# Optimization experiments

Hardware: AMD Instinct MI355X
Metric: run time of the kernel (lower is better)

## Reference

```python
import jax, jax.numpy as jnp
import numpy as np
from jax import lax

EPS = 1e-5
DN = ('NCHW', 'OIHW', 'NCHW')


def _bn(x, gamma, beta, mean, var):
    # eval-mode BatchNorm2d over channel dim (axis=1)
    s = gamma / jnp.sqrt(var + EPS)
    return x * s[None, :, None, None] + (beta - mean * s)[None, :, None, None]


def setup_inputs() -> dict:
    key = jax.random.key(0)
    ks = jax.random.split(key, 12)
    B, Cin, C, H, W, NC = 128, 2048, 512, 14, 14, 200
    return {
        'feature': jax.random.normal(ks[0], (B, Cin, H, W), jnp.float32),
        'w_reduce': jax.random.normal(ks[1], (C, Cin, 1, 1), jnp.float32) * 0.02,
        'b_reduce': jax.random.normal(ks[2], (C,), jnp.float32) * 0.02,
        'bn1_gamma': jnp.ones((C,), jnp.float32),
        'bn1_beta': jnp.zeros((C,), jnp.float32),
        'bn1_mean': jax.random.normal(ks[3], (C,), jnp.float32) * 0.02,
        'bn1_var': jax.random.uniform(ks[4], (C,), jnp.float32),
        'w3': jax.random.normal(ks[5], (C, C, 3, 3), jnp.float32) * 0.02,
        'b3': jax.random.normal(ks[6], (C,), jnp.float32) * 0.02,
        'bn2_gamma': jnp.ones((C,), jnp.float32),
        'bn2_beta': jnp.zeros((C,), jnp.float32),
        'bn2_mean': jax.random.normal(ks[7], (C,), jnp.float32) * 0.02,
        'bn2_var': jax.random.uniform(ks[8], (C,), jnp.float32),
        'fc1_w': jax.random.normal(ks[9], (NC, C), jnp.float32) * 0.02,
        'fc1_b': jnp.zeros((NC,), jnp.float32),
        'fc2_w': jax.random.normal(ks[10], (NC, NC), jnp.float32) * 0.02,
        'fc2_b': jnp.zeros((NC,), jnp.float32),
    }


def reference(feature, w_reduce, b_reduce, bn1_gamma, bn1_beta, bn1_mean, bn1_var,
              w3, b3, bn2_gamma, bn2_beta, bn2_mean, bn2_var,
              fc1_w, fc1_b, fc2_w, fc2_b):
    B, _, H, W = feature.shape
    C = w_reduce.shape[0]  # 512
    # reduce: 1x1 conv + BN + ReLU
    f = lax.conv_general_dilated(feature, w_reduce, (1, 1), 'VALID', dimension_numbers=DN)
    f = f + b_reduce[None, :, None, None]
    f = jax.nn.relu(_bn(f, bn1_gamma, bn1_beta, bn1_mean, bn1_var))
    x = f.reshape(B, C, H * W)  # [B, 512, 196]
    # channel affinity + softmax(-xxt) over last dim (= the per-row loop)
    xxt = jnp.einsum('bcn,bdn->bcd', x, x)  # [B, 512, 512]
    a = jax.nn.softmax(-xxt, axis=2)
    y = jnp.einsum('bcd,bdn->bcn', a, x).reshape(B, C, H, W)
    # conv3: 3x3 conv + BN + ReLU + global avg pool
    z = lax.conv_general_dilated(y, w3, (1, 1), 'SAME', dimension_numbers=DN)
    z = z + b3[None, :, None, None]
    z = jax.nn.relu(_bn(z, bn2_gamma, bn2_beta, bn2_mean, bn2_var))
    z = jnp.mean(z, axis=(2, 3))  # [B, 512]
    # fc_channel: Linear -> ReLU -> Linear
    h = jax.nn.relu(z @ fc1_w.T + fc1_b)
    sf = h @ fc2_w.T + fc2_b
    return sf
```

## Files before the change

### kernel.cpp

```cpp
#include <hip/hip_runtime.h>

typedef __attribute__((ext_vector_type(8))) short bf16x8;
typedef __attribute__((ext_vector_type(4))) float f32x4;
typedef __attribute__((ext_vector_type(4))) short short4v;
typedef __attribute__((ext_vector_type(2))) short short2v;

__device__ __forceinline__ unsigned short f2bf(float x){
  unsigned u = __float_as_uint(x);
  return (unsigned short)((u + 0x7FFFu + ((u>>16)&1u)) >> 16);
}
__device__ __forceinline__ float bf2f(unsigned short b){
  return __uint_as_float(((unsigned)b)<<16);
}

typedef const __attribute__((address_space(1))) void* gas_t;
typedef __attribute__((address_space(3))) void* las_t;
__device__ __forceinline__ void gl16(const void* g, void* l){
  __builtin_amdgcn_global_load_lds((gas_t)g, (las_t)l, 16, 0, 0);
}

static constexpr size_t O_FHI  = 0;
static constexpr size_t O_FLO  = 102760448;
static constexpr size_t O_XHI  = 205520896;
static constexpr size_t O_XLO  = 239075328;
static constexpr size_t O_XT   = 272629760;
static constexpr size_t O_AMAT = 301989888;
static constexpr size_t O_WH   = 369098752;
static constexpr size_t O_WL   = 371195904;
static constexpr size_t O_W3B  = 373293056;
static constexpr size_t O_PAR  = 378011648;
static constexpr size_t O_FC1T = 378019840;
static constexpr size_t O_FC2T = 378429440;
static constexpr size_t O_ZBAR = 378589440;

__global__ __launch_bounds__(256) void k_prep(
    const float* wr, unsigned short* wh, unsigned short* wl,
    const float* w3, unsigned short* w3c,
    const float* fc1w, float* fc1T, const float* fc2w, float* fc2T,
    const float* br, const float* g1, const float* be1, const float* m1, const float* v1,
    const float* b3, const float* g2, const float* be2, const float* m2, const float* v2,
    float* par, unsigned short* xhi, unsigned short* xlo){
  int blk = blockIdx.x, t = threadIdx.x;
  if (blk < 4096){
    int idx = blk*256 + t;
    int c = idx >> 11, k = idx & 2047;
    float v = wr[(size_t)c*2048 + k];
    unsigned short h = f2bf(v);
    wh[(size_t)c*2048+k] = h; wl[(size_t)c*2048+k] = f2bf(v - bf2f(h));
  } else if (blk < 13312){
    int i = (blk-4096)*256 + t;
    int co = i / 4608, k = i - co*4608;
    int ci0b = k / 576, r2 = k - ci0b*576;
    int tap = r2 >> 6, cio = r2 & 63;
    w3c[(((size_t)ci0b*9+tap)*512+co)*64+cio] =
        f2bf(w3[((size_t)co*512 + ci0b*64+cio)*9 + tap]);
  } else if (blk < 13712){
    int i = (blk-13312)*256 + t;
    int k = i/200, j = i - k*200;
    fc1T[i] = fc1w[j*512+k];
  } else if (blk < 13869){
    int i = (blk-13712)*256 + t;
    if (i < 40000){ int k = i/200, j = i - k*200; fc2T[i] = fc2w[j*200+k]; }
  } else if (blk < 13871){
    int c = (blk-13869)*256 + t;
    if (c < 512){
      float s1 = g1[c]*rsqrtf(v1[c]+1e-5f);
      par[c] = s1; par[512+c] = (br[c]-m1[c])*s1 + be1[c];
      float s2 = g2[c]*rsqrtf(v2[c]+1e-5f);
      par[1024+c] = s2; par[1536+c] = (b3[c]-m2[c])*s2 + be2[c];
    }
  } else {
    int rr = (blk-13871)*256 + t;
    float4 z = {0.f,0.f,0.f,0.f};
    float4* a = (float4*)(xhi + (size_t)rr*256 + 192);
    float4* bq = (float4*)(xlo + (size_t)rr*256 + 192);
    #pragma unroll
    for (int q=0;q<8;++q){ a[q]=z; bq[q]=z; }
  }
}

__global__ __launch_bounds__(256) void k_featT(const float* __restrict__ feat,
        unsigned short* __restrict__ fhi, unsigned short* __restrict__ flo){
  __shared__ float tile[64][33];
  int b = blockIdx.z;
  int ci0 = blockIdx.y*64, p0 = blockIdx.x*32;
  int t = threadIdx.x;
  int j = t & 31, i0 = t >> 5;
  for (int rep=0; rep<8; ++rep){
    int i = rep*8 + i0;
    int p = p0 + j;
    tile[i][j] = (p<196) ? feat[((size_t)b*2048 + ci0 + i)*196 + p] : 0.f;
  }
  __syncthreads();
  int j2 = t & 31;
  int jj0 = t >> 5;
  for (int rep=0; rep<4; ++rep){
    int jj = rep*8 + jj0;
    int p = p0 + jj;
    if (p < 196){
      float v0 = tile[2*j2][jj], v1 = tile[2*j2+1][jj];
      unsigned short h0 = f2bf(v0), h1 = f2bf(v1);
      unsigned short l0 = f2bf(v0 - bf2f(h0)), l1 = f2bf(v1 - bf2f(h1));
      size_t o = ((size_t)b*196 + p)*2048 + ci0 + 2*j2;
      short2v hv; hv[0]=(short)h0; hv[1]=(short)h1;
      short2v lv; lv[0]=(short)l0; lv[1]=(short)l1;
      *(short2v*)(fhi + o) = hv;
      *(short2v*)(flo + o) = lv;
    }
  }
}

__global__ __launch_bounds__(256, 2) void k_conv1(
    const unsigned short* __restrict__ fhi, const unsigned short* __restrict__ flo,
    const unsigned short* __restrict__ wh,  const unsigned short* __restrict__ wl,
    const float* __restrict__ par,
    unsigned short* __restrict__ xhi, unsigned short* __restrict__ xlo,
    unsigned short* __restrict__ xT){
  __shared__ char lds[65536];
  char* BUF0 = lds;
  char* BUF1 = lds + 32768;
  int lin = blockIdx.x;
  int sz  = (lin&7)*98 + (lin>>3);
  int mt = sz&3;
  int gt = sz>>2;
  int c0 = mt*128;
  size_t g0 = (size_t)gt*128;
  int t = threadIdx.x, lane = t&63, wid = t>>6, wm = wid&1, wn = wid>>1;
  int fq = lane>>4, fr = lane&15;
  f32x4 acc[4][4] = {};

  auto STAGE = [&](int it, char* buf){
    #pragma unroll
    for (int jj=0; jj<8; ++jj){
      int arr = jj>>1;
      int g = t + ((jj&1)<<8);
      int row = g>>2;
      int cs = ((g&3) ^ ((row>>1)&3))*8;
      const unsigned short* src;
      if (arr==0)      src = wh  + (size_t)(c0+row)*2048 + it*32 + cs;
      else if (arr==1) src = wl  + (size_t)(c0+row)*2048 + it*32 + cs;
      else if (arr==2) src = fhi + (g0+row)*2048 + it*32 + cs;
      else             src = flo + (g0+row)*2048 + it*32 + cs;
      gl16(src, buf + arr*8192 + g*16);
    }
  };

  STAGE(0, BUF0);
  asm volatile("s_waitcnt vmcnt(0)" ::: "memory");
  __builtin_amdgcn_s_barrier();
  __builtin_amdgcn_sched_barrier(0);

  for (int it=0; it<64; ++it){
    char* cur = (it&1) ? BUF1 : BUF0;
    char* nxt = (it&1) ? BUF0 : BUF1;
    if (it < 63) STAGE(it+1, nxt);
    bf16x8 ah[4], al[4], bh[4], bl[4];
    #pragma unroll
    for (int m=0;m<4;++m){
      int row = wm*64 + m*16 + fr;
      int off = row*64 + ((fq*16) ^ (((row>>1)&3)<<4));
      ah[m] = *(const bf16x8*)(cur + off);
      al[m] = *(const bf16x8*)(cur + 8192 + off);
    }
    #pragma unroll
    for (int n=0;n<4;++n){
      int row = wn*64 + n*16 + fr;
      int off = row*64 + ((fq*16) ^ (((row>>1)&3)<<4));
      bh[n] = *(const bf16x8*)(cur + 16384 + off);
      bl[n] = *(const bf16x8*)(cur + 24576 + off);
    }
    __builtin_amdgcn_s_setprio(1);
    #pragma unroll
    for (int n=0;n<4;++n)
      #pragma unroll
      for (int m=0;m<4;++m){
        acc[m][n] = __builtin_amdgcn_mfma_f32_16x16x32_bf16(ah[m], bh[n], acc[m][n],0,0,0);
        acc[m][n] = __builtin_amdgcn_mfma_f32_16x16x32_bf16(ah[m], bl[n], acc[m][n],0,0,0);
        acc[m][n] = __builtin_amdgcn_mfma_f32_16x16x32_bf16(al[m], bh[n], acc[m][n],0,0,0);
      }
    __builtin_amdgcn_s_setprio(0);
    asm volatile("s_waitcnt vmcnt(0)" ::: "memory");
    __builtin_amdgcn_s_barrier();
    __builtin_amdgcn_sched_barrier(0);
  }

  const float* s1 = par; const float* t1 = par+512;
  for (int m=0;m<4;++m){
    int cb = c0 + wm*64 + m*16 + fq*4;
    float sc[4], sh[4];
    for (int j=0;j<4;++j){ sc[j]=s1[cb+j]; sh[j]=t1[cb+j]; }
    for (int n=0;n<4;++n){
      int gg = (int)g0 + wn*64 + n*16 + fr;
      int b = gg/196, p = gg - b*196;
      unsigned short hs[4];
      for (int j=0;j<4;++j){
        float v = fmaxf(acc[m][n][j]*sc[j]+sh[j], 0.f);
        unsigned short h = f2bf(v);
        hs[j] = h;
        size_t ic = (size_t)b*512 + cb + j;
        xhi[ic*256 + p] = h;
        xlo[ic*256 + p] = f2bf(v - bf2f(h));
      }
      *(short4v*)(xT + ((size_t)b*224 + p)*512 + cb) = *(short4v*)hs;
    }
  }
}

__global__ __launch_bounds__(256) void k_xxt(const unsigned short* __restrict__ xhi,
        const unsigned short* __restrict__ xlo, float* __restrict__ xxt){
  __shared__ char lds[32768];
  char* Als = lds; char* Bls = lds + 16384;
  int lin = blockIdx.x;
  int sz  = (lin&7)*160 + (lin>>3);
  int b = sz/10, sub = sz - b*10;
  unsigned mtp = (3u<<18)|(2u<<16)|(2u<<14)|(1u<<12)|(1u<<10)|(1u<<8)|(0u<<6)|(0u<<4)|(0u<<2)|0u;
  unsigned ntp = (3u<<18)|(3u<<16)|(2u<<14)|(3u<<12)|(2u<<10)|(1u<<8)|(3u<<6)|(2u<<4)|(1u<<2)|0u;
  int mt = (mtp>>(2*sub))&3, nt = (ntp>>(2*sub))&3;
  int c0 = mt*128, d0 = nt*128;
  int t = threadIdx.x, lane = t&63, wid = t>>6, wm = wid&1, wn = wid>>1;
  int fq = lane>>4, fr = lane&15;
  f32x4 acc[4][4] = {};
  for (int it=0; it<12; ++it){
    int seg = it>>2, kk0 = (it&3)*64;
    const unsigned short* As = (seg<2) ? xhi : xlo;
    const unsigned short* Bs = (seg==1) ? xlo : xhi;
    __syncthreads();
    #pragma unroll
    for (int r=0;r<4;++r){
      int L = r*256 + t;
      int row = L>>3, cs = ((L&7)^(row&7))*8;
      gl16(As + ((size_t)b*512 + c0 + row)*256 + kk0 + cs, Als + L*16);
      gl16(Bs + ((size_t)b*512 + d0 + row)*256 + kk0 + cs, Bls + L*16);
    }
    __syncthreads();
    #pragma unroll
    for (int ks=0; ks<2; ++ks){
      int kb = ks*64 + fq*16;
      bf16x8 af[4];
      #pragma unroll
      for (int m=0;m<4;++m){
        int row = wm*64 + m*16 + fr;
        af[m] = *(const bf16x8*)(Als + row*128 + (kb ^ ((row&7)<<4)));
      }
      #pragma unroll
      for (int n=0;n<4;++n){
        int row = wn*64 + n*16 + fr;
        bf16x8 bff = *(const bf16x8*)(Bls + row*128 + (kb ^ ((row&7)<<4)));
        #pragma unroll
        for (int m=0;m<4;++m)
          acc[m][n] = __builtin_amdgcn_mfma_f32_16x16x32_bf16(af[m], bff, acc[m][n],0,0,0);
      }
    }
  }
  for (int m=0;m<4;++m){
    int cb = c0 + wm*64 + m*16 + fq*4;
    for (int n=0;n<4;++n){
      int d = d0 + wn*64 + n*16 + fr;
      *(float4*)(xxt + ((size_t)b*512 + d)*512 + cb) = *(float4*)&acc[m][n];
    }
  }
  if (mt != nt){
    for (int m=0;m<4;++m){
      int cb = c0 + wm*64 + m*16 + fq*4;
      for (int n=0;n<4;++n){
        int d = d0 + wn*64 + n*16 + fr;
        for (int jj=0;jj<4;++jj)
          xxt[((size_t)b*512 + cb + jj)*512 + d] = acc[m][n][jj];
      }
    }
  }
}

__global__ __launch_bounds__(256) void k_softmax(const float* __restrict__ xxt, unsigned short* __restrict__ amat){
  int row = blockIdx.x*4 + (threadIdx.x>>6);
  int lane = threadIdx.x & 63;
  const float* src = xxt + (size_t)row*512 + lane*8;
  float4 v0 = *(const float4*)src;
  float4 v1 = *(const float4*)(src+4);
  float mn = fminf(fminf(fminf(v0.x,v0.y),fminf(v0.z,v0.w)),
                   fminf(fminf(v1.x,v1.y),fminf(v1.z,v1.w)));
  for (int m=32; m; m>>=1) mn = fminf(mn, __shfl_xor(mn, m, 64));
  float e[8];
  e[0]=__expf(mn-v0.x); e[1]=__expf(mn-v0.y); e[2]=__expf(mn-v0.z); e[3]=__expf(mn-v0.w);
  e[4]=__expf(mn-v1.x); e[5]=__expf(mn-v1.y); e[6]=__expf(mn-v1.z); e[7]=__expf(mn-v1.w);
  float s = e[0]+e[1]+e[2]+e[3]+e[4]+e[5]+e[6]+e[7];
  for (int m=32; m; m>>=1) s += __shfl_xor(s, m, 64);
  float inv = 1.f/s;
  short4v p0, p1;
  for (int q=0;q<4;++q) p0[q] = (short)f2bf(e[q]*inv);
  for (int q=0;q<4;++q) p1[q] = (short)f2bf(e[4+q]*inv);
  unsigned short* dst = amat + (size_t)row*512 + lane*8;
  *(short4v*)dst = p0;
  *(short4v*)(dst+4) = p1;
}

__global__ __launch_bounds__(256) void k_pv(const unsigned short* __restrict__ amat,
        const unsigned short* __restrict__ xT, unsigned short* __restrict__ ypad){
  __shared__ char lds[30720];
  char* Als = lds; char* Bls = lds + 16384;
  int lin = blockIdx.x, per = gridDim.x>>3;
  int sz  = (lin&7)*per + (lin>>3);
  int b = sz>>3, sub = sz&7, mt = sub>>1, nt = sub&1;
  int c0 = mt*128, n0 = nt*112;
  int t = threadIdx.x, lane = t&63, wid = t>>6;
  int fq = lane>>4, fr = lane&15;
  {
    int r = t;
    int hi = r>>4, lo2 = r&15;
    if (hi==0||hi==15||lo2==0||lo2==15){
      float4 z = {0.f,0.f,0.f,0.f};
      float4* pz = (float4*)(ypad + (((size_t)b*8 + sub)*256 + r)*64);
      #pragma unroll
      for (int q=0;q<8;++q) pz[q] = z;
    }
  }
  f32x4 acc[2][7] = {};
  for (int it=0; it<8; ++it){
    int k0 = it*64;
    __syncthreads();
    #pragma unroll
    for (int r=0;r<4;++r){
      int L = r*256 + t;
      int row = L>>3, cs = ((L&7)^(row&7))*8;
      gl16(amat + ((size_t)b*512 + c0 + row)*512 + k0 + cs, Als + L*16);
    }
    #pragma unroll
    for (int r=0;r<4;++r){
      int L = r*256 + t;
      if (L < 896){
        int row = L>>3, cs = ((L&7)^(row&7))*8;
        gl16(xT + ((size_t)b*224 + n0 + row)*512 + k0 + cs, Bls + L*16);
      }
    }
    __syncthreads();
    #pragma unroll
    for (int ks=0; ks<2; ++ks){
      int kb = ks*64 + fq*16;
      bf16x8 af[2];
      #pragma unroll
      for (int m=0;m<2;++m){
        int row = wid*32 + m*16 + fr;
        af[m] = *(const bf16x8*)(Als + row*128 + (kb ^ ((row&7)<<4)));
      }
      #pragma unroll
      for (int n=0;n<7;++n){
        int row = n*16 + fr;
        bf16x8 bff = *(const bf16x8*)(Bls + row*128 + (kb ^ ((row&7)<<4)));
        #pragma unroll
        for (int m=0;m<2;++m)
          acc[m][n] = __builtin_amdgcn_mfma_f32_16x16x32_bf16(af[m], bff, acc[m][n],0,0,0);
      }
    }
  }
  for (int m=0;m<2;++m){
    int cb = c0 + wid*32 + m*16 + fq*4;
    int ci0b = cb>>6, cio = cb&63;
    for (int n=0;n<7;++n){
      int p = n0 + n*16 + fr;
      if (p < 196){
        int hh = p/14, wwp = p - hh*14;
        int prow = (hh+1)*16 + (wwp+1);
        short4v pk;
        for (int j=0;j<4;++j) pk[j] = (short)f2bf(acc[m][n][j]);
        *(short4v*)(ypad + (((size_t)b*8 + ci0b)*256 + prow)*64 + cio) = pk;
      }
    }
  }
}

__global__ __launch_bounds__(512, 2) void k_conv3(const unsigned short* __restrict__ ypad,
        const unsigned short* __restrict__ w3c, const float* __restrict__ par,
        float* __restrict__ zbar){
  __shared__ char lds[65536];
  char* WIN = lds;
  char* AB0 = lds + 32768;
  char* AB1 = lds + 49152;
  int bx = blockIdx.x;
  int xcd = bx&7, jj2 = bx>>3;
  int b = xcd*16 + (jj2>>2), cot = jj2&3;
  int c0 = cot*128;
  int t = threadIdx.x, lane = t&63, w = t>>6;
  int wm = w>>2, wn = (w>>1)&1, wks = w&1;
  int fq = lane>>4, fr = lane&15;
  int frB = (fr<14) ? fr : 13;
  bool pok = (fr<14);
  f32x4 acc[4][7] = {};
  for (int ci0=0; ci0<8; ++ci0){
    const unsigned short* wsrc = ypad + ((size_t)(b*8 + ci0)*256)*64;
    #pragma unroll
    for (int r=0;r<4;++r){
      int L = r*512 + t;
      int row = L>>3, cs = ((L&7)^(row&7))*8;
      gl16(wsrc + row*64 + cs, WIN + L*16);
    }
    {
      const unsigned short* asrc = w3c + ((size_t)(ci0*9 + 0)*512 + c0)*64;
      #pragma unroll
      for (int r=0;r<2;++r){
        int L = r*512 + t;
        int row = L>>3, cs = ((L&7)^(row&7))*8;
        gl16(asrc + row*64 + cs, AB0 + L*16);
      }
    }
    __syncthreads();
    for (int tap=0; tap<9; ++tap){
      char* Acur = (tap&1) ? AB1 : AB0;
      char* Anxt = (tap&1) ? AB0 : AB1;
      if (tap < 8){
        const unsigned short* asrc = w3c + ((size_t)(ci0*9 + tap+1)*512 + c0)*64;
        #pragma unroll
        for (int r=0;r<2;++r){
          int L = r*512 + t;
          int row = L>>3, cs = ((L&7)^(row&7))*8;
          gl16(asrc + row*64 + cs, Anxt + L*16);
        }
      }
      int kh = tap/3, kw = tap - kh*3;
      bf16x8 ah[4];
      #pragma unroll
      for (int m=0;m<4;++m){
        int row = wm*64 + m*16 + fr;
        ah[m] = *(const bf16x8*)(Acur + row*128 + (((wks*4+fq)^(row&7))<<4));
      }
      int col = frB + kw;
      __builtin_amdgcn_s_setprio(1);
      #pragma unroll
      for (int n=0;n<7;++n){
        int prow = (wn*7 + n + kh)*16 + col;
        bf16x8 bf = *(const bf16x8*)(WIN + prow*128 + (((wks*4+fq)^(prow&7))<<4));
        #pragma unroll
        for (int m=0;m<4;++m)
          acc[m][n] = __builtin_amdgcn_mfma_f32_16x16x32_bf16(ah[m], bf, acc[m][n],0,0,0);
      }
      __builtin_amdgcn_s_setprio(0);
      __syncthreads();
    }
  }
  #pragma unroll
  for (int half=0; half<2; ++half){
    if (wks){
      #pragma unroll
      for (int m2=0;m2<2;++m2)
        #pragma unroll
        for (int n=0;n<7;++n)
          *(f32x4*)(lds + (((size_t)((wm*2+wn)*14 + m2*7 + n))*64 + lane)*16) = acc[half*2+m2][n];
    }
    __syncthreads();
    if (!wks){
      #pragma unroll
      for (int m2=0;m2<2;++m2)
        #pragma unroll
        for (int n=0;n<7;++n){
          f32x4 o = *(const f32x4*)(lds + (((size_t)((wm*2+wn)*14 + m2*7 + n))*64 + lane)*16);
          acc[half*2+m2][n] += o;
        }
    }
    __syncthreads();
  }
  const float* s2 = par+1024; const float* t2 = par+1536;
  float ps[4][4];
  if (!wks){
    #pragma unroll
    for (int m=0;m<4;++m){
      int cb = c0 + wm*64 + m*16 + fq*4;
      #pragma unroll
      for (int j=0;j<4;++j){
        float sc = s2[cb+j], sh = t2[cb+j];
        float s = 0.f;
        #pragma unroll
        for (int n=0;n<7;++n)
          s += fmaxf(acc[m][n][j]*sc + sh, 0.f);
        ps[m][j] = pok ? s : 0.f;
      }
    }
    #pragma unroll
    for (int off=1; off<16; off<<=1)
      #pragma unroll
      for (int m=0;m<4;++m)
        #pragma unroll
        for (int j=0;j<4;++j)
          ps[m][j] += __shfl_xor(ps[m][j], off, 64);
  }
  float* part = (float*)lds;
  if (!wks && fr == 0){
    #pragma unroll
    for (int m=0;m<4;++m)
      #pragma unroll
      for (int j=0;j<4;++j)
        part[wn*128 + wm*64 + m*16 + fq*4 + j] = ps[m][j];
  }
  __syncthreads();
  if (t < 128)
    zbar[(size_t)b*512 + c0 + t] = part[t] + part[128 + t];
}

__global__ __launch_bounds__(256) void k_fc(const float* __restrict__ zbar,
        const float* __restrict__ fc1T, const float* __restrict__ fc1b,
        const float* __restrict__ fc2T, const float* __restrict__ fc2b,
        float* __restrict__ out){
  __shared__ float zb[512];
  __shared__ float hl[200];
  int b = blockIdx.x, t = threadIdx.x;
  zb[t]     = zbar[(size_t)b*512 + t]       * (1.f/196.f);
  zb[t+256] = zbar[(size_t)b*512 + t + 256] * (1.f/196.f);
  __syncthreads();
  if (t < 200){
    float acc = fc1b[t];
    for (int k=0;k<512;++k) acc += zb[k]*fc1T[k*200+t];
    hl[t] = fmaxf(acc, 0.f);
  }
  __syncthreads();
  if (t < 200){
    float acc = fc2b[t];
    for (int k=0;k<200;++k) acc += hl[k]*fc2T[k*200+t];
    out[(size_t)b*200 + t] = acc;
  }
}

extern "C" void kernel_launch(void* const* d_in, const int* in_sizes, int n_in,
                              void* d_out, int out_size, void* d_ws, size_t ws_size,
                              hipStream_t stream) {
  const float* feature  = (const float*)d_in[0];
  const float* w_reduce = (const float*)d_in[1];
  const float* b_reduce = (const float*)d_in[2];
  const float* g1  = (const float*)d_in[3];
  const float* be1 = (const float*)d_in[4];
  const float* m1  = (const float*)d_in[5];
  const float* v1  = (const float*)d_in[6];
  const float* w3  = (const float*)d_in[7];
  const float* b3  = (const float*)d_in[8];
  const float* g2  = (const float*)d_in[9];
  const float* be2 = (const float*)d_in[10];
  const float* m2  = (const float*)d_in[11];
  const float* v2  = (const float*)d_in[12];
  const float* fc1w = (const float*)d_in[13];
  const float* fc1b = (const float*)d_in[14];
  const float* fc2w = (const float*)d_in[15];
  const float* fc2b = (const float*)d_in[16];

  char* ws = (char*)d_ws;
  unsigned short* fhi  = (unsigned short*)(ws + O_FHI);
  unsigned short* flo  = (unsigned short*)(ws + O_FLO);
  float*          xxt  = (float*)(ws + O_FHI);
  unsigned short* xhi  = (unsigned short*)(ws + O_XHI);
  unsigned short* xlo  = (unsigned short*)(ws + O_XLO);
  unsigned short* ypad = (unsigned short*)(ws + O_XLO);
  unsigned short* xT   = (unsigned short*)(ws + O_XT);
  unsigned short* amat = (unsigned short*)(ws + O_AMAT);
  unsigned short* wh   = (unsigned short*)(ws + O_WH);
  unsigned short* wl   = (unsigned short*)(ws + O_WL);
  unsigned short* w3c  = (unsigned short*)(ws + O_W3B);
  float* par  = (float*)(ws + O_PAR);
  float* fc1T = (float*)(ws + O_FC1T);
  float* fc2T = (float*)(ws + O_FC2T);
  float* zbar = (float*)(ws + O_ZBAR);

  k_prep<<<14127, 256, 0, stream>>>(w_reduce, wh, wl, w3, w3c,
      fc1w, fc1T, fc2w, fc2T,
      b_reduce, g1, be1, m1, v1, b3, g2, be2, m2, v2, par, xhi, xlo);

  k_featT<<<dim3(7,32,128), 256, 0, stream>>>(feature, fhi, flo);
  k_conv1<<<784, 256, 0, stream>>>(fhi, flo, wh, wl, par, xhi, xlo, xT);

  k_xxt<<<1280, 256, 0, stream>>>(xhi, xlo, xxt);
  k_softmax<<<16384, 256, 0, stream>>>(xxt, amat);

  k_pv<<<1024, 256, 0, stream>>>(amat, xT, ypad);
  k_conv3<<<512, 512, 0, stream>>>(ypad, w3c, par, zbar);
  k_fc<<<128, 256, 0, stream>>>(zbar, fc1T, fc1b, fc2T, fc2b, (float*)d_out);
}
```

Baseline: 593.3 us.

## Split reduce-GEMM staging into two phases with partial waits

The 1x1-conv GEMM stage is split so the next tile's flo operand is issued after the other three operands. The MFMA loop is divided into two halves: the first uses wh/wl/fhi and waits only on vmcnt(2), and the ah*bl products run after a second barrier. The aim is to overlap global-to-LDS loads with compute rather than draining all loads at the end of each iteration. The cost is an extra barrier per iteration and more fragile vmcnt accounting.

```diff
diff --git a/kernel.cpp b/kernel.cpp
--- a/kernel.cpp
+++ b/kernel.cpp
@@ -129,9 +129,9 @@
   int fq = lane>>4, fr = lane&15;
   f32x4 acc[4][4] = {};
 
-  auto STAGE = [&](int it, char* buf){
-    #pragma unroll
-    for (int jj=0; jj<8; ++jj){
+  auto STAGE1 = [&](int it, char* buf){
+    #pragma unroll
+    for (int jj=0; jj<6; ++jj){
       int arr = jj>>1;
       int g = t + ((jj&1)<<8);
       int row = g>>2;
@@ -139,22 +139,30 @@
       const unsigned short* src;
       if (arr==0)      src = wh  + (size_t)(c0+row)*2048 + it*32 + cs;
       else if (arr==1) src = wl  + (size_t)(c0+row)*2048 + it*32 + cs;
-      else if (arr==2) src = fhi + (g0+row)*2048 + it*32 + cs;
-      else             src = flo + (g0+row)*2048 + it*32 + cs;
+      else             src = fhi + (g0+row)*2048 + it*32 + cs;
       gl16(src, buf + arr*8192 + g*16);
     }
   };
-
-  STAGE(0, BUF0);
-  asm volatile("s_waitcnt vmcnt(0)" ::: "memory");
-  __builtin_amdgcn_s_barrier();
-  __builtin_amdgcn_sched_barrier(0);
+  auto STAGE2 = [&](int it, char* buf){
+    #pragma unroll
+    for (int jj=0; jj<2; ++jj){
+      int g = t + (jj<<8);
+      int row = g>>2;
+      int cs = ((g&3) ^ ((row>>1)&3))*8;
+      gl16(flo + (g0+row)*2048 + it*32 + cs, buf + 24576 + g*16);
+    }
+  };
+
+  STAGE1(0, BUF0);
+  STAGE2(0, BUF0);
 
   for (int it=0; it<64; ++it){
     char* cur = (it&1) ? BUF1 : BUF0;
     char* nxt = (it&1) ? BUF0 : BUF1;
-    if (it < 63) STAGE(it+1, nxt);
-    bf16x8 ah[4], al[4], bh[4], bl[4];
+    asm volatile("s_waitcnt vmcnt(2)" ::: "memory");
+    __builtin_amdgcn_s_barrier();
+    __builtin_amdgcn_sched_barrier(0);
+    bf16x8 ah[4], al[4], bh[4];
     #pragma unroll
     for (int m=0;m<4;++m){
       int row = wm*64 + m*16 + fr;
@@ -167,21 +175,40 @@
       int row = wn*64 + n*16 + fr;
       int off = row*64 + ((fq*16) ^ (((row>>1)&3)<<4));
       bh[n] = *(const bf16x8*)(cur + 16384 + off);
-      bl[n] = *(const bf16x8*)(cur + 24576 + off);
-    }
+    }
+    if (it < 63) STAGE1(it+1, nxt);
+    asm volatile("s_waitcnt lgkmcnt(0)" ::: "memory");
+    __builtin_amdgcn_sched_barrier(0);
     __builtin_amdgcn_s_setprio(1);
     #pragma unroll
     for (int n=0;n<4;++n)
       #pragma unroll
       for (int m=0;m<4;++m){
         acc[m][n] = __builtin_amdgcn_mfma_f32_16x16x32_bf16(ah[m], bh[n], acc[m][n],0,0,0);
-        acc[m][n] = __builtin_amdgcn_mfma_f32_16x16x32_bf16(ah[m], bl[n], acc[m][n],0,0,0);
         acc[m][n] = __builtin_amdgcn_mfma_f32_16x16x32_bf16(al[m], bh[n], acc[m][n],0,0,0);
       }
     __builtin_amdgcn_s_setprio(0);
-    asm volatile("s_waitcnt vmcnt(0)" ::: "memory");
+    if (it < 63) { asm volatile("s_waitcnt vmcnt(6)" ::: "memory"); }
+    else         { asm volatile("s_waitcnt vmcnt(0)" ::: "memory"); }
     __builtin_amdgcn_s_barrier();
     __builtin_amdgcn_sched_barrier(0);
+    bf16x8 bl[4];
+    #pragma unroll
+    for (int n=0;n<4;++n){
+      int row = wn*64 + n*16 + fr;
+      int off = row*64 + ((fq*16) ^ (((row>>1)&3)<<4));
+      bl[n] = *(const bf16x8*)(cur + 24576 + off);
+    }
+    if (it < 63) STAGE2(it+1, nxt);
+    asm volatile("s_waitcnt lgkmcnt(0)" ::: "memory");
+    __builtin_amdgcn_sched_barrier(0);
+    __builtin_amdgcn_s_setprio(1);
+    #pragma unroll
+    for (int n=0;n<4;++n)
+      #pragma unroll
+      for (int m=0;m<4;++m)
+        acc[m][n] = __builtin_amdgcn_mfma_f32_16x16x32_bf16(ah[m], bl[n], acc[m][n],0,0,0);
+    __builtin_amdgcn_s_setprio(0);
   }
 
   const float* s1 = par; const float* t1 = par+512;
```

New measurement: 606.9 us. 2.3% more time.
